# Performance work log

Hardware: AMD Instinct MI355X
Metric: run time of the kernel (lower is better)

## Reference

```python
import jax, jax.numpy as jnp
import numpy as np

K = 128          # num_clusters (init kwarg k)
N_ITERS = 100    # torch loop runs up to 100 iters; converged centroids are a
                 # fixed point, so running all 100 matches the early-exit result


def _sq_dists(x, c):
    # squared Euclidean distances [N, K]; argmin identical to torch.cdist argmin
    return (jnp.sum(x * x, axis=1, keepdims=True)
            - 2.0 * (x @ c.T)
            + jnp.sum(c * c, axis=1)[None, :])


def _assign_and_update(x, c):
    ids = jnp.argmin(_sq_dists(x, c), axis=1)                     # [N]
    sums = jax.ops.segment_sum(x, ids, num_segments=K)            # [K, D]
    counts = jax.ops.segment_sum(jnp.ones((x.shape[0],), x.dtype), ids,
                                 num_segments=K)                  # [K]
    return ids, sums / counts[:, None]   # mean per cluster (NaN if empty, as in torch)


def setup_inputs() -> dict:
    key = jax.random.key(0)
    kx, kp = jax.random.split(key)
    N, D = 32768, 256
    x = jax.random.normal(kx, (N, D), dtype=jnp.float32)
    # torch.randperm(N)[:K] -> distinct initial centroid indices
    init_idx = jax.random.permutation(kp, N)[:K].astype(jnp.int32)
    return {"x": x, "init_idx": init_idx}


def reference(x, init_idx):
    c0 = x[init_idx]  # [K, D]

    def body(c, _):
        _, newc = _assign_and_update(x, c)
        return newc, None

    # 99 updates, then final assignment + update: returned ids correspond to the
    # centroids BEFORE the last update, exactly like the torch loop's last iter.
    c, _ = jax.lax.scan(body, c0, None, length=N_ITERS - 1)
    ids, c = _assign_and_update(x, c)

    logits = x @ c.T  # temperature = 1.0
    logp = jax.nn.log_softmax(logits, axis=-1)
    # CrossEntropyLoss(mean) with pseudo labels = cluster ids
    loss = -jnp.mean(jnp.take_along_axis(logp, ids[:, None], axis=1))
    return loss
```

## Files before the change

### kernel.cpp

```cpp
#include <hip/hip_runtime.h>
#include <cstdint>

#define NPTS 32768
#define DIM  256
#define NK   128
#define NITER 100
#define NBLK 256
#define NTHR 1024
#define PAD  33

typedef unsigned short ushort_t;
typedef unsigned long long ull_t;
typedef __attribute__((ext_vector_type(8))) short s8v;
typedef __attribute__((ext_vector_type(4))) float f4v;

__device__ __forceinline__ unsigned short f2bf(float f) {
  unsigned u = __float_as_uint(f);
  u += 0x7fffu + ((u >> 16) & 1u);
  return (unsigned short)(u >> 16);
}
__device__ __forceinline__ float bf2f(unsigned short b) {
  return __uint_as_float(((unsigned)b) << 16);
}

__device__ __forceinline__ void cstore(float* p, float v) {
  __hip_atomic_store(p, v, __ATOMIC_RELAXED, __HIP_MEMORY_SCOPE_AGENT);
}
__device__ __forceinline__ float cload(const float* p) {
  return __hip_atomic_load(p, __ATOMIC_RELAXED, __HIP_MEMORY_SCOPE_AGENT);
}
__device__ __forceinline__ void cstorei(int* p, int v) {
  __hip_atomic_store(p, v, __ATOMIC_RELAXED, __HIP_MEMORY_SCOPE_AGENT);
}
__device__ __forceinline__ int cloadi(const int* p) {
  return __hip_atomic_load(p, __ATOMIC_RELAXED, __HIP_MEMORY_SCOPE_AGENT);
}
__device__ __forceinline__ void cstore64(ull_t* p, ull_t v) {
  __hip_atomic_store(p, v, __ATOMIC_RELAXED, __HIP_MEMORY_SCOPE_AGENT);
}

__device__ __forceinline__ void gbar(unsigned* flags, unsigned* grep, unsigned gen) {
  __syncthreads();
  if (threadIdx.x == 0)
    __hip_atomic_store(&flags[blockIdx.x * 16], gen, __ATOMIC_RELAXED, __HIP_MEMORY_SCOPE_AGENT);
  if (blockIdx.x == 0) {
    if (threadIdx.x < NBLK) {
      while (__hip_atomic_load(&flags[threadIdx.x * 16], __ATOMIC_RELAXED, __HIP_MEMORY_SCOPE_AGENT) < gen)
        __builtin_amdgcn_s_sleep(2);
    }
    __syncthreads();
    if (threadIdx.x < 64)
      __hip_atomic_store(&grep[threadIdx.x * 16], gen, __ATOMIC_RELAXED, __HIP_MEMORY_SCOPE_AGENT);
  }
  if (threadIdx.x == 0) {
    while (__hip_atomic_load(&grep[(blockIdx.x & 63) * 16], __ATOMIC_RELAXED, __HIP_MEMORY_SCOPE_AGENT) < gen)
      __builtin_amdgcn_s_sleep(2);
  }
  __syncthreads();
  asm volatile("" ::: "memory");
  __syncthreads();
}

union StU {
  struct { char ch[128 * 80]; char cl[128 * 80]; } a;
  struct { float accB[NK * PAD]; ushort_t idsl16[1024]; } b;
  struct { float red4[1024]; float redcn[1024]; } c;
};

__device__ __forceinline__ void gemm_core(
    const s8v* __restrict__ xhR, const s8v* __restrict__ xlR,
    StU& u, float* cns, int t,
    const ull_t* __restrict__ cpk, const float* __restrict__ cn2, f4v (&acc)[2][2]) {
  const int lane = t & 63;
  const int w    = t >> 6;
  const int wr   = w >> 2, wc = w & 3;
  const int g    = lane >> 4, lr = lane & 15;

  if (t < NK) cns[t] = cload(&cn2[2 * t]) + cload(&cn2[2 * t + 1]);

  const f4v zero = {0.f, 0.f, 0.f, 0.f};
#pragma unroll
  for (int i = 0; i < 2; ++i)
#pragma unroll
    for (int j = 0; j < 2; ++j) acc[i][j] = zero;

  for (int q = 0; q < 8; ++q) {
    if (t < 512) {
      int row = t >> 2, c = t & 3;
      const ull_t* src = cpk + (size_t)row * 128 + q * 16 + c * 4;
      ull_t w0 = src[0], w1 = src[1], w2 = src[2], w3 = src[3];
      s8v vh, vl;
      vh[0] = (short)w0; vl[0] = (short)(w0 >> 16); vh[1] = (short)(w0 >> 32); vl[1] = (short)(w0 >> 48);
      vh[2] = (short)w1; vl[2] = (short)(w1 >> 16); vh[3] = (short)(w1 >> 32); vl[3] = (short)(w1 >> 48);
      vh[4] = (short)w2; vl[4] = (short)(w2 >> 16); vh[5] = (short)(w2 >> 32); vl[5] = (short)(w2 >> 48);
      vh[6] = (short)w3; vl[6] = (short)(w3 >> 16); vh[7] = (short)(w3 >> 32); vl[7] = (short)(w3 >> 48);
      *(s8v*)(u.a.ch + row * 80 + c * 16) = vh;
      *(s8v*)(u.a.cl + row * 80 + c * 16) = vl;
    }
    __syncthreads();
    s8v ah[2], al[2], bh[2], bl[2];
#pragma unroll
    for (int i = 0; i < 2; ++i) {
      int ra = wr * 32 + i * 16 + lr;
      int o = ra * 512 + (((q * 4 + g) ^ (lr & 7)) * 16);
      ah[i] = *(const s8v*)((const char*)xhR + o);
      al[i] = *(const s8v*)((const char*)xlR + o);
    }
#pragma unroll
    for (int j = 0; j < 2; ++j) {
      int rb = wc * 32 + j * 16 + lr;
      int o = rb * 80 + g * 16;
      bh[j] = *(const s8v*)(u.a.ch + o);
      bl[j] = *(const s8v*)(u.a.cl + o);
    }
#pragma unroll
    for (int i = 0; i < 2; ++i)
#pragma unroll
      for (int j = 0; j < 2; ++j) {
        acc[i][j] = __builtin_amdgcn_mfma_f32_16x16x32_bf16(ah[i], bh[j], acc[i][j], 0, 0, 0);
        acc[i][j] = __builtin_amdgcn_mfma_f32_16x16x32_bf16(ah[i], bl[j], acc[i][j], 0, 0, 0);
        acc[i][j] = __builtin_amdgcn_mfma_f32_16x16x32_bf16(al[i], bh[j], acc[i][j], 0, 0, 0);
      }
    __syncthreads();
  }
}

__global__ __launch_bounds__(NTHR, 1) void kmeans_fused(
    const float* __restrict__ x, const int* __restrict__ init_idx,
    ull_t* __restrict__ cpkv, float* __restrict__ cn2v, int* __restrict__ ids,
    float* __restrict__ psum, float* __restrict__ pcnt,
    float* __restrict__ outp, unsigned* __restrict__ flags,
    unsigned* __restrict__ grep, float* __restrict__ out) {
  __shared__ s8v xhR[4096];
  __shared__ s8v xlR[4096];
  __shared__ StU u;
  __shared__ float cns[NK];
  __shared__ float redd[NK * 4];
  __shared__ int   redk[NK * 4];
  __shared__ float gmaxs[NK];
  __shared__ float labvs[NK];
  __shared__ int   labis[NK];
  __shared__ int   cntB[NK];
  __shared__ ushort_t hsm[DIM], lsm[DIM];
  __shared__ float cntsh;

  const int b = blockIdx.x;
  const int t = threadIdx.x;
  const int lane = t & 63;
  const int w  = t >> 6;
  const int wr = w >> 2, wc = w & 3;
  const int g  = lane >> 4, lr = lane & 15;
  const int pbase = b * 128;
  unsigned gen = 1;

  for (int i = 0; i < 4; ++i) {
    int G = i * NTHR + t;
    int row = G >> 5, c = G & 31;
    const float4* src = (const float4*)(x + ((size_t)pbase + row) * DIM + c * 8);
    float4 fa = src[0], fb = src[1];
    float vv[8] = {fa.x, fa.y, fa.z, fa.w, fb.x, fb.y, fb.z, fb.w};
    s8v vh, vl;
#pragma unroll
    for (int j = 0; j < 8; ++j) {
      unsigned short hh = f2bf(vv[j]);
      vh[j] = (short)hh;
      vl[j] = (short)f2bf(vv[j] - bf2f(hh));
    }
    int pos = c ^ (row & 7);
    *(s8v*)((char*)xhR + row * 512 + pos * 16) = vh;
    *(s8v*)((char*)xlR + row * 512 + pos * 16) = vl;
  }

  if (b < NK) {
    float eff = 0.f;
    if (t < DIM) {
      float v = x[init_idx[b] * DIM + t];
      unsigned short hh = f2bf(v);
      unsigned short ll = f2bf(v - bf2f(hh));
      hsm[t] = hh; lsm[t] = ll;
      eff = bf2f(hh) + bf2f(ll);
    }
    __syncthreads();
    u.c.redcn[t] = (t < DIM) ? eff * eff : 0.f;
    if (t < NK) {
      ull_t wv = (ull_t)hsm[2 * t] | ((ull_t)lsm[2 * t] << 16)
               | ((ull_t)hsm[2 * t + 1] << 32) | ((ull_t)lsm[2 * t + 1] << 48);
      cstore64(&cpkv[(size_t)b * 128 + t], wv);
    }
    __syncthreads();
    for (int s = 512; s > 0; s >>= 1) { if (t < s) u.c.redcn[t] += u.c.redcn[t + s]; __syncthreads(); }
    if (t == 0) { cstore(&cn2v[b * 2], u.c.redcn[0]); cstore(&cn2v[b * 2 + 1], 0.f); }
  }
  gbar(flags, grep, gen); ++gen;
  if (t == 0) __threadfence();
  __syncthreads();

  for (int it = 0; it < NITER; ++it) {
    const ull_t*  cpkR = cpkv + (size_t)it * (NK * 128);
    const float*  cn2R = cn2v + (size_t)it * (NK * 2);
    ull_t* cpkW = cpkv + (size_t)(it + 1) * (NK * 128);
    float* cn2W = cn2v + (size_t)(it + 1) * (NK * 2);

    {
      f4v acc[2][2];
      gemm_core(xhR, xlR, u, cns, t, cpkR, cn2R, acc);
#pragma unroll
      for (int i = 0; i < 2; ++i) {
#pragma unroll
        for (int r = 0; r < 4; ++r) {
          int prow = wr * 32 + i * 16 + g * 4 + r;
          float bd = 1e30f; int bk = 0;
#pragma unroll
          for (int j = 0; j < 2; ++j) {
            int col = wc * 32 + j * 16 + lr;
            float s = cns[col] - 2.f * acc[i][j][r];
            if (s < bd || (s == bd && col < bk)) { bd = s; bk = col; }
          }
#pragma unroll
          for (int msk = 1; msk < 16; msk <<= 1) {
            float od = __shfl_xor(bd, msk, 64);
            int   ok = __shfl_xor(bk, msk, 64);
            if (od < bd || (od == bd && ok < bk)) { bd = od; bk = ok; }
          }
          if (lr == 0) { redd[prow * 4 + wc] = bd; redk[prow * 4 + wc] = bk; }
        }
      }
      __syncthreads();
      if (t < NK) {
        float bd = redd[t * 4]; int bk = redk[t * 4];
#pragma unroll
        for (int q = 1; q < 4; ++q) {
          float dq = redd[t * 4 + q]; int kq = redk[t * 4 + q];
          if (dq < bd || (dq == bd && kq < bk)) { bd = dq; bk = kq; }
        }
        cstorei(&ids[pbase + t], bk);
      }
    }
    gbar(flags, grep, gen); ++gen;

    {
      const int pg = b & 31, dg = b >> 5;
      for (int i = t; i < NK * PAD; i += NTHR) u.b.accB[i] = 0.f;
      if (t < NK) cntB[t] = 0;
      u.b.idsl16[t] = (ushort_t)cloadi(&ids[pg * 1024 + t]);
      __syncthreads();
      const int id = u.b.idsl16[t];
      if (dg == 0) atomicAdd(&cntB[id], 1);
      const float4* xr = (const float4*)(x + ((size_t)pg * 1024 + t) * DIM + dg * 32);
      float4 v0 = xr[0], v1 = xr[1], v2 = xr[2], v3 = xr[3];
      float4 v4 = xr[4], v5 = xr[5], v6 = xr[6], v7 = xr[7];
      float* ab = &u.b.accB[id * PAD];
      atomicAdd(ab + 0,  v0.x); atomicAdd(ab + 1,  v0.y); atomicAdd(ab + 2,  v0.z); atomicAdd(ab + 3,  v0.w);
      atomicAdd(ab + 4,  v1.x); atomicAdd(ab + 5,  v1.y); atomicAdd(ab + 6,  v1.z); atomicAdd(ab + 7,  v1.w);
      atomicAdd(ab + 8,  v2.x); atomicAdd(ab + 9,  v2.y); atomicAdd(ab + 10, v2.z); atomicAdd(ab + 11, v2.w);
      atomicAdd(ab + 12, v3.x); atomicAdd(ab + 13, v3.y); atomicAdd(ab + 14, v3.z); atomicAdd(ab + 15, v3.w);
      atomicAdd(ab + 16, v4.x); atomicAdd(ab + 17, v4.y); atomicAdd(ab + 18, v4.z); atomicAdd(ab + 19, v4.w);
      atomicAdd(ab + 20, v5.x); atomicAdd(ab + 21, v5.y); atomicAdd(ab + 22, v5.z); atomicAdd(ab + 23, v5.w);
      atomicAdd(ab + 24, v6.x); atomicAdd(ab + 25, v6.y); atomicAdd(ab + 26, v6.z); atomicAdd(ab + 27, v6.w);
      atomicAdd(ab + 28, v7.x); atomicAdd(ab + 29, v7.y); atomicAdd(ab + 30, v7.z); atomicAdd(ab + 31, v7.w);
      __syncthreads();
#pragma unroll
      for (int s2 = 0; s2 < 4; ++s2) {
        int idx = s2 * NTHR + t;
        int k2 = idx >> 5, dl = idx & 31;
        cstore(&psum[(((size_t)dg * NK + k2) * 32 + pg) * 32 + dl], u.b.accB[k2 * PAD + dl]);
      }
      if (dg == 0 && t < NK)
        cstore(&pcnt[(size_t)pg * NK + t], (float)cntB[t]);
    }
    gbar(flags, grep, gen); ++gen;

    {
      const int k = b >> 1, hh2 = b & 1;
      const int dwh = t & 127, pch = t >> 7;
      const int dgc = hh2 * 4 + (dwh >> 5), dlc = dwh & 31;
      float s = 0.f;
#pragma unroll
      for (int p2 = pch * 4; p2 < pch * 4 + 4; ++p2)
        s += cload(&psum[(((size_t)dgc * NK + k) * 32 + p2) * 32 + dlc]);
      u.c.red4[pch * 128 + dwh] = s;
      float cv = (t < 32) ? cload(&pcnt[(size_t)t * NK + k]) : 0.f;
      if (t < 64) {
#pragma unroll
        for (int m = 1; m < 32; m <<= 1) cv += __shfl_xor(cv, m, 64);
      }
      if (t == 0) cntsh = cv;
      __syncthreads();
      float eff = 0.f;
      if (t < 128) {
        float ssum = 0.f;
#pragma unroll
        for (int ww = 0; ww < 8; ++ww) ssum += u.c.red4[ww * 128 + t];
        float mean = ssum / cntsh;
        unsigned short hh = f2bf(mean);
        unsigned short ll = f2bf(mean - bf2f(hh));
        hsm[t] = hh; lsm[t] = ll;
        eff = bf2f(hh) + bf2f(ll);
      }
      __syncthreads();
      u.c.redcn[t] = (t < 128) ? eff * eff : 0.f;
      if (t < 64) {
        ull_t wv = (ull_t)hsm[2 * t] | ((ull_t)lsm[2 * t] << 16)
                 | ((ull_t)hsm[2 * t + 1] << 32) | ((ull_t)lsm[2 * t + 1] << 48);
        cstore64(&cpkW[(size_t)k * 128 + hh2 * 64 + t], wv);
      }
      __syncthreads();
      for (int st = 512; st > 0; st >>= 1) { if (t < st) u.c.redcn[t] += u.c.redcn[t + st]; __syncthreads(); }
      if (t == 0) cstore(&cn2W[k * 2 + hh2], u.c.redcn[0]);
    }
    gbar(flags, grep, gen); ++gen;
  }

  {
    f4v acc[2][2];
    gemm_core(xhR, xlR, u, cns, t,
              cpkv + (size_t)NITER * (NK * 128), cn2v + (size_t)NITER * (NK * 2), acc);
#pragma unroll
    for (int i = 0; i < 2; ++i) {
#pragma unroll
      for (int r = 0; r < 4; ++r) {
        int prow = wr * 32 + i * 16 + g * 4 + r;
        float m = -1e30f;
#pragma unroll
        for (int j = 0; j < 2; ++j) m = fmaxf(m, acc[i][j][r]);
#pragma unroll
        for (int msk = 1; msk < 16; msk <<= 1) m = fmaxf(m, __shfl_xor(m, msk, 64));
        if (lr == 0) redd[prow * 4 + wc] = m;
      }
    }
    __syncthreads();
    if (t < NK) {
      float m = redd[t * 4];
#pragma unroll
      for (int q = 1; q < 4; ++q) m = fmaxf(m, redd[t * 4 + q]);
      gmaxs[t] = m;
      labis[t] = cloadi(&ids[pbase + t]);
    }
    __syncthreads();
#pragma unroll
    for (int i = 0; i < 2; ++i) {
#pragma unroll
      for (int r = 0; r < 4; ++r) {
        int prow = wr * 32 + i * 16 + g * 4 + r;
        float m = gmaxs[prow];
        int lab = labis[prow];
        float s = 0.f;
#pragma unroll
        for (int j = 0; j < 2; ++j) {
          int col = wc * 32 + j * 16 + lr;
          float v = acc[i][j][r];
          s += expf(v - m);
          if (col == lab) labvs[prow] = v;
        }
#pragma unroll
        for (int msk = 1; msk < 16; msk <<= 1) s += __shfl_xor(s, msk, 64);
        if (lr == 0) redd[prow * 4 + wc] = s;
      }
    }
    __syncthreads();
    if (t < NK) {
      float se = redd[t * 4] + redd[t * 4 + 1] + redd[t * 4 + 2] + redd[t * 4 + 3];
      float lse = gmaxs[t] + logf(se);
      gmaxs[t] = lse - labvs[t];
    }
    __syncthreads();
    if (t == 0) {
      float tot = 0.f;
      for (int q = 0; q < NK; ++q) tot += gmaxs[q];
      cstore(&outp[b], tot);
    }
  }
  gbar(flags, grep, gen); ++gen;
  if (b == 0) {
    u.c.redcn[t] = (t < NBLK) ? cload(&outp[t]) : 0.f;
    __syncthreads();
    for (int s = 512; s > 0; s >>= 1) { if (t < s) u.c.redcn[t] += u.c.redcn[t + s]; __syncthreads(); }
    if (t == 0) out[0] = u.c.redcn[0] * (1.0f / (float)NPTS);
  }
}

extern "C" void kernel_launch(void* const* d_in, const int* in_sizes, int n_in,
                              void* d_out, int out_size, void* d_ws, size_t ws_size,
                              hipStream_t stream) {
  const float* x        = (const float*)d_in[0];
  const int*   init_idx = (const int*)d_in[1];
  float* out = (float*)d_out;
  char* ws = (char*)d_ws;

  ull_t* cpkv = (ull_t*)(ws);
  float* cn2v = (float*)(ws + 13238272);
  int*   ids  = (int*)(ws + 13341696);
  float* psum = (float*)(ws + 13472768);
  float* pcnt = (float*)(ws + 17667072);
  float* outp = (float*)(ws + 17683456);
  unsigned* flags = (unsigned*)(ws + 17684480);
  unsigned* grep  = (unsigned*)(ws + 17700864);

  hipMemsetAsync(flags, 0, 20480, stream);
  kmeans_fused<<<dim3(NBLK), dim3(NTHR), 0, stream>>>(
      x, init_idx, cpkv, cn2v, ids, psum, pcnt, outp, flags, grep, out);
}
```

Baseline: 6.861 ms.

## Remap segment-sum LDS atomics so lanes span dims and write partials as 64-bit stores

The per-cluster sum stage used to give each thread one point and have it issue 32 LDS atomics to consecutive dims of that point's cluster row. Now each wavefront walks its 64 points two at a time, with lanes indexing the dimension. The cluster id is broadcast by shuffle and x is read with coalesced per-lane loads. This spreads same-instant atomics across distinct dims, meant to cut LDS bank conflicts and same-address serialization. The partial-sum writeback is also packed into 64-bit stores, halving the store instruction count. The cost is more loop iterations, scalar instead of float4 global loads, and a shuffle per step.

```diff
diff --git a/kernel.cpp b/kernel.cpp
--- a/kernel.cpp
+++ b/kernel.cpp
@@ -244,26 +244,27 @@
       if (t < NK) cntB[t] = 0;
       u.b.idsl16[t] = (ushort_t)cloadi(&ids[pg * 1024 + t]);
       __syncthreads();
-      const int id = u.b.idsl16[t];
-      if (dg == 0) atomicAdd(&cntB[id], 1);
-      const float4* xr = (const float4*)(x + ((size_t)pg * 1024 + t) * DIM + dg * 32);
-      float4 v0 = xr[0], v1 = xr[1], v2 = xr[2], v3 = xr[3];
-      float4 v4 = xr[4], v5 = xr[5], v6 = xr[6], v7 = xr[7];
-      float* ab = &u.b.accB[id * PAD];
-      atomicAdd(ab + 0,  v0.x); atomicAdd(ab + 1,  v0.y); atomicAdd(ab + 2,  v0.z); atomicAdd(ab + 3,  v0.w);
-      atomicAdd(ab + 4,  v1.x); atomicAdd(ab + 5,  v1.y); atomicAdd(ab + 6,  v1.z); atomicAdd(ab + 7,  v1.w);
-      atomicAdd(ab + 8,  v2.x); atomicAdd(ab + 9,  v2.y); atomicAdd(ab + 10, v2.z); atomicAdd(ab + 11, v2.w);
-      atomicAdd(ab + 12, v3.x); atomicAdd(ab + 13, v3.y); atomicAdd(ab + 14, v3.z); atomicAdd(ab + 15, v3.w);
-      atomicAdd(ab + 16, v4.x); atomicAdd(ab + 17, v4.y); atomicAdd(ab + 18, v4.z); atomicAdd(ab + 19, v4.w);
-      atomicAdd(ab + 20, v5.x); atomicAdd(ab + 21, v5.y); atomicAdd(ab + 22, v5.z); atomicAdd(ab + 23, v5.w);
-      atomicAdd(ab + 24, v6.x); atomicAdd(ab + 25, v6.y); atomicAdd(ab + 26, v6.z); atomicAdd(ab + 27, v6.w);
-      atomicAdd(ab + 28, v7.x); atomicAdd(ab + 29, v7.y); atomicAdd(ab + 30, v7.z); atomicAdd(ab + 31, v7.w);
-      __syncthreads();
-#pragma unroll
-      for (int s2 = 0; s2 < 4; ++s2) {
+      const int wbase = w * 64;
+      const int hh = lane >> 5, d = lane & 31;
+      const int myid = u.b.idsl16[wbase + lane];
+      if (dg == 0) atomicAdd(&cntB[myid], 1);
+      const float* xb = x + ((size_t)pg * 1024 + wbase) * DIM + dg * 32;
+#pragma unroll 4
+      for (int s = 0; s < 32; ++s) {
+        int p2 = s * 2 + hh;
+        int id = __shfl(myid, p2, 64);
+        float v = xb[(size_t)p2 * DIM + d];
+        atomicAdd(&u.b.accB[id * PAD + d], v);
+      }
+      __syncthreads();
+#pragma unroll
+      for (int s2 = 0; s2 < 2; ++s2) {
         int idx = s2 * NTHR + t;
-        int k2 = idx >> 5, dl = idx & 31;
-        cstore(&psum[(((size_t)dg * NK + k2) * 32 + pg) * 32 + dl], u.b.accB[k2 * PAD + dl]);
+        int k2 = idx >> 4, dl2 = idx & 15;
+        float lo = u.b.accB[k2 * PAD + dl2 * 2];
+        float hi2 = u.b.accB[k2 * PAD + dl2 * 2 + 1];
+        ull_t pv = (ull_t)__float_as_uint(lo) | ((ull_t)__float_as_uint(hi2) << 32);
+        cstore64((ull_t*)&psum[(((size_t)dg * NK + k2) * 32 + pg) * 32 + dl2 * 2], pv);
       }
       if (dg == 0 && t < NK)
         cstore(&pcnt[(size_t)pg * NK + t], (float)cntB[t]);
```

After: 6.973 ms. No clear change (+1.6%).
